# Kernel tuning notes

Measured on AMD Instinct MI355X. Metric: run time of the kernel, lower is better.

## Reference

```python
import jax, jax.numpy as jnp
import numpy as np

B = 1; T = 2048; H = 2048; NH = 16; KVH = 4; HD = 128; WIN = 512; SINK = 64
S = 64; NG = 4; MLP_I = 5504; CK = 4
INTER = NH * HD; CONV_DIM = INTER + 2 * NG * S; NPROJ = INTER + CONV_DIM + NH
EPS = 1e-6; MEPS = 1e-5


def rmsnorm(x, w, eps):
    return x * jax.lax.rsqrt(jnp.mean(x * x, -1, keepdims=True) + eps) * w


def rotate_half(x):
    h = x.shape[-1] // 2
    return jnp.concatenate([-x[..., h:], x[..., :h]], -1)


def setup_inputs():
    key = jax.random.key(0)
    ks = jax.random.split(key, 32)
    rn = lambda k, s, sc=0.02: jax.random.normal(k, s, dtype=jnp.float32) * sc
    inv = 1.0 / (10000.0 ** (np.arange(0, HD, 2, dtype=np.float64) / HD))
    fr = np.outer(np.arange(T), inv)
    emb = np.concatenate([fr, fr], -1)
    return {
        'hidden_states': jax.random.normal(ks[0], (B, T, H), dtype=jnp.float32),
        'cos': jnp.asarray(np.cos(emb), jnp.float32)[None],
        'sin': jnp.asarray(np.sin(emb), jnp.float32)[None],
        'ln1_w': jnp.ones((H,), jnp.float32),
        'q_w': rn(ks[1], (NH * HD, H)), 'q_b': rn(ks[2], (NH * HD,)),
        'k_w': rn(ks[3], (KVH * HD, H)), 'k_b': rn(ks[4], (KVH * HD,)),
        'v_w': rn(ks[5], (KVH * HD, H)), 'v_b': rn(ks[6], (KVH * HD,)),
        'o_w': rn(ks[7], (H, NH * HD)),
        'in_proj_w': rn(ks[8], (NPROJ, H)),
        'conv_w': rn(ks[9], (CONV_DIM, 1, CK), 0.1),
        'conv_b': rn(ks[10], (CONV_DIM,), 0.1),
        'dt_bias': rn(ks[11], (NH,), 0.5),
        'A_log': rn(ks[12], (NH,), 0.5),
        'D': rn(ks[13], (NH,), 0.5),
        'mnorm_w': jnp.ones((INTER,), jnp.float32),
        'out_proj_w': rn(ks[14], (H, INTER)),
        'ln2_w': jnp.ones((H,), jnp.float32),
        'gate_w': rn(ks[15], (MLP_I, H)),
        'up_w': rn(ks[16], (MLP_I, H)),
        'down_w': rn(ks[17], (H, MLP_I)),
    }


def _mamba2(ev, in_proj_w, conv_w, conv_b, dt_bias, A_log, D, mnorm_w, out_proj_w):
    # ev: [B, L, H] evicted hidden states; Mamba2 with expand=1 (intermediate=INTER)
    L = ev.shape[1]
    proj = jnp.einsum('blh,ph->blp', ev, in_proj_w)
    z = proj[..., :INTER]
    xBC = proj[..., INTER:INTER + CONV_DIM]
    dt = proj[..., INTER + CONV_DIM:]
    # depthwise causal conv1d, kernel 4
    xBC = jax.lax.conv_general_dilated(
        xBC.transpose(0, 2, 1), conv_w, (1,), [(CK - 1, 0)],
        dimension_numbers=('NCH', 'OIH', 'NCH'), feature_group_count=CONV_DIM)
    xBC = jax.nn.silu((xBC + conv_b[None, :, None]).transpose(0, 2, 1))
    x = xBC[..., :INTER].reshape(B, L, NH, HD)
    Bm = jnp.repeat(xBC[..., INTER:INTER + NG * S].reshape(B, L, NG, S), NH // NG, axis=2)
    Cm = jnp.repeat(xBC[..., INTER + NG * S:].reshape(B, L, NG, S), NH // NG, axis=2)
    dt = jax.nn.softplus(dt + dt_bias)  # [B, L, NH]
    A = -jnp.exp(A_log)  # [NH]

    def scan_one(xb, bb, cb, db):
        def step(state, inp):
            xt, bt, ct, dtt = inp  # [NH,HD],[NH,S],[NH,S],[NH]
            decay = jnp.exp(dtt * A)[:, None, None]
            state = decay * state + (dtt[:, None] * xt)[..., None] * bt[:, None, :]
            y = jnp.einsum('hds,hs->hd', state, ct) + D[:, None] * xt
            return state, y
        _, ys = jax.lax.scan(step, jnp.zeros((NH, HD, S), xb.dtype), (xb, bb, cb, db))
        return ys

    y = jax.vmap(scan_one)(x, Bm, Cm, dt).reshape(B, L, INTER)
    g = y * jax.nn.silu(z)  # gated RMSNorm
    g = g * jax.lax.rsqrt(jnp.mean(g * g, -1, keepdims=True) + MEPS) * mnorm_w
    return jnp.einsum('bli,hi->blh', g, out_proj_w)


def reference(hidden_states, cos, sin, ln1_w, q_w, q_b, k_w, k_b, v_w, v_b, o_w,
              in_proj_w, conv_w, conv_b, dt_bias, A_log, D, mnorm_w, out_proj_w,
              ln2_w, gate_w, up_w, down_w):
    pre = rmsnorm(hidden_states, ln1_w, EPS)  # input_layernorm
    evict_end = T - WIN
    mem_out = _mamba2(pre[:, SINK:evict_end, :], in_proj_w, conv_w, conv_b,
                      dt_bias, A_log, D, mnorm_w, out_proj_w)  # [B, Le, H]
    mem_act = mem_out[:, -1:, :]

    def qkv(x, w, b, nh):
        return (jnp.einsum('blh,ph->blp', x, w) + b).reshape(x.shape[0], x.shape[1], nh, HD).transpose(0, 2, 1, 3)

    q = qkv(pre, q_w, q_b, NH)
    k = qkv(pre, k_w, k_b, KVH)
    v = qkv(pre, v_w, v_b, KVH)
    c = cos[:, None]; s = sin[:, None]
    q = q * c + rotate_half(q) * s
    k = k * c + rotate_half(k) * s
    # mem token injection at position SINK (mem projections are not rotated)
    q = q.at[:, :, SINK, :].set(qkv(mem_act, q_w, q_b, NH)[:, :, 0, :])
    k = k.at[:, :, SINK, :].set(qkv(mem_act, k_w, k_b, KVH)[:, :, 0, :])
    v = v.at[:, :, SINK, :].set(qkv(mem_act, v_w, v_b, KVH)[:, :, 0, :])
    # sink + sliding-window causal mask with mem-token bias
    row = jnp.arange(T)[:, None]; col = jnp.arange(T)[None, :]
    protected = SINK + 1
    bad = (col > row) | ((col < row - WIN) & (col >= protected))
    minv = jnp.finfo(jnp.float32).min
    mask = jnp.where(bad, minv, 0.0)[None, None]
    le_fact = (T - SINK - WIN) / T
    mask = mask.at[..., SINK].add(0.5 * le_fact)
    rep = NH // KVH
    kf = jnp.repeat(k, rep, axis=1)
    vf = jnp.repeat(v, rep, axis=1)
    scores = jnp.einsum('bhqd,bhkd->bhqk', q, kf) * (HD ** -0.5) + mask
    attn = jax.nn.softmax(scores, axis=-1)
    o = jnp.einsum('bhqk,bhkd->bhqd', attn, vf).transpose(0, 2, 1, 3).reshape(B, T, NH * HD)
    # training-path merge: sinks | mem_out | window
    merged = jnp.concatenate([o[:, :SINK], mem_out, o[:, T - WIN:]], axis=1)
    attn_out = jnp.einsum('blp,hp->blh', merged, o_w)
    h = hidden_states + attn_out
    m = rmsnorm(h, ln2_w, EPS)
    mlp = jnp.einsum('bli,hi->blh',
                     jax.nn.silu(jnp.einsum('blh,ih->bli', m, gate_w)) * jnp.einsum('blh,ih->bli', m, up_w),
                     down_w)
    return h + mlp
```

## Files before the change

### kernel.cpp

```cpp
#include <hip/hip_runtime.h>
#include <hip/hip_bf16.h>

#define TSEQ   2048
#define HDIM   2048
#define NHEAD  16
#define KVHEAD 4
#define HEADD  128
#define WINSZ  512
#define SINKN  64
#define MLPI   5504
#define CONVD  2560
#define NPROJD 4624
#define LMEM   1472
#define NCHUNK 23
#define QKVD   3072

typedef unsigned short bf_t;
typedef __attribute__((ext_vector_type(8))) short short8;
typedef __attribute__((ext_vector_type(4))) short s4v;
typedef __attribute__((ext_vector_type(4))) float ffrag;

#define BOF_PRE   0ull
#define BOF_QKV   8388608ull
#define BOF_P     8388608ull
#define BOF_S     20447232ull
#define BOF_PROJ  33554432ull
#define BOF_GB    33554432ull
#define BOF_XBCC  60780544ull
#define BOF_GF    75853824ull
#define BOF_MERG  75853824ull
#define BOF_GN    87912448ull
#define BOF_H     93941760ull
#define BOF_DT    110718976ull
#define BOF_GA    110813184ull
#define BOF_FLAG  110907392ull
#define BOF_LC    110908416ull

#define BOF_CNV_A 8388608ull
#define BOF_CNV_B 60780544ull

__device__ __forceinline__ float bf2f(bf_t x) { return __uint_as_float(((unsigned)x) << 16); }
__device__ __forceinline__ bf_t f2bf(float x) {
  unsigned u = __float_as_uint(x);
  return (bf_t)((u + 0x7FFFu + ((u >> 16) & 1u)) >> 16);
}
__device__ __forceinline__ float ldin(const void* p, size_t i, int bf) {
  if (bf) return bf2f(((const bf_t*)p)[i]);
  return ((const float*)p)[i];
}
__device__ __forceinline__ float siluf(float x) { return x / (1.f + expf(-x)); }

typedef const __attribute__((address_space(1))) unsigned gl_u32;
typedef __attribute__((address_space(3))) unsigned lds_u32;
__device__ __forceinline__ void gld16(const void* g, void* l) {
  __builtin_amdgcn_global_load_lds((gl_u32*)g, (lds_u32*)l, 16, 0, 0);
}

__device__ __forceinline__ void xcd_swz(int gx, int gy, int& x, int& y) {
  int id = blockIdx.y * gx + blockIdx.x;
  int total = gx * gy;
  int xcd = id & 7, j = id >> 3;
  int q = total >> 3, r = total & 7;
  int w = (xcd < r ? xcd*(q+1) : r*(q+1) + (xcd-r)*q) + j;
  x = w / gy;
  y = w % gy;
}

__global__ void detect_k(const void* __restrict__ ln1, int* __restrict__ flag) {
  unsigned w0 = *(const unsigned*)ln1;
  *flag = (w0 == 0x3F803F80u) ? 1 : 0;
}

__global__ __launch_bounds__(256) void wconv_k(const float* __restrict__ src,
    bf_t* __restrict__ dst, int n8, const int* __restrict__ flagp) {
  if (*flagp) return;
  int idx = blockIdx.x*256 + threadIdx.x;
  if (idx >= n8) return;
  const float* s = src + (size_t)idx*8;
  float4 a = *(const float4*)s, b = *(const float4*)(s+4);
  short8 o;
  o[0]=(short)f2bf(a.x); o[1]=(short)f2bf(a.y); o[2]=(short)f2bf(a.z); o[3]=(short)f2bf(a.w);
  o[4]=(short)f2bf(b.x); o[5]=(short)f2bf(b.y); o[6]=(short)f2bf(b.z); o[7]=(short)f2bf(b.w);
  *(short8*)(dst + (size_t)idx*8) = o;
}

__global__ __launch_bounds__(256) void rms_in_k(const void* __restrict__ x,
    const void* __restrict__ w, bf_t* __restrict__ out, float eps,
    const int* __restrict__ flagp) {
  int bf = *flagp;
  int row = blockIdx.x, tid = threadIdx.x;
  float v[8];
  if (bf) {
    const bf_t* xr = (const bf_t*)x + (size_t)row*HDIM + tid*8;
#pragma unroll
    for (int j = 0; j < 8; ++j) v[j] = bf2f(xr[j]);
  } else {
    const float* xr = (const float*)x + (size_t)row*HDIM + tid*8;
    float4 a = *(const float4*)xr, b = *(const float4*)(xr+4);
    v[0]=a.x; v[1]=a.y; v[2]=a.z; v[3]=a.w; v[4]=b.x; v[5]=b.y; v[6]=b.z; v[7]=b.w;
  }
  float ss = 0.f;
#pragma unroll
  for (int j = 0; j < 8; ++j) ss += v[j]*v[j];
  __shared__ float red[256];
  red[tid] = ss; __syncthreads();
  for (int s = 128; s > 0; s >>= 1) { if (tid < s) red[tid] += red[tid+s]; __syncthreads(); }
  float scale = 1.f / sqrtf(red[0]*(1.f/HDIM) + eps);
  bf_t* o = out + (size_t)row*HDIM + tid*8;
#pragma unroll
  for (int j = 0; j < 8; ++j) o[j] = f2bf(v[j]*scale*ldin(w, tid*8+j, bf));
}

__global__ __launch_bounds__(256) void rms_f2b_k(const float* __restrict__ x,
    const void* __restrict__ w, bf_t* __restrict__ out, float eps,
    const int* __restrict__ flagp) {
  int bf = *flagp;
  int row = blockIdx.x, tid = threadIdx.x;
  const float* xr = x + (size_t)row*2048 + tid*8;
  float4 a = *(const float4*)xr, b = *(const float4*)(xr+4);
  float v[8] = {a.x,a.y,a.z,a.w,b.x,b.y,b.z,b.w};
  float ss = 0.f;
#pragma unroll
  for (int j = 0; j < 8; ++j) ss += v[j]*v[j];
  __shared__ float red[256];
  red[tid] = ss; __syncthreads();
  for (int s = 128; s > 0; s >>= 1) { if (tid < s) red[tid] += red[tid+s]; __syncthreads(); }
  float scale = 1.f / sqrtf(red[0]*(1.f/2048.f) + eps);
  bf_t* o = out + (size_t)row*2048 + tid*8;
#pragma unroll
  for (int j = 0; j < 8; ++j) o[j] = f2bf(v[j]*scale*ldin(w, tid*8+j, bf));
}

__global__ __launch_bounds__(256) void tgemm_k(
    const bf_t* __restrict__ A, int lda,
    const void* __restrict__ W0, const void* __restrict__ W1, const void* __restrict__ W2,
    const bf_t* __restrict__ C0, const bf_t* __restrict__ C1, const bf_t* __restrict__ C2,
    int ldw, int n1, int n2,
    const void* __restrict__ b0, const void* __restrict__ b1, const void* __restrict__ b2,
    const void* __restrict__ res,
    const float* __restrict__ hf,
    void* __restrict__ out,
    int ldc, int M, int N, int K, int mode, int outbf,
    const int* __restrict__ flagp) {
  int bf = *flagp;
  __shared__ short As[8192];
  __shared__ short Bs[4096];
  int tid = threadIdx.x;
  int lane = tid & 63, wv = tid >> 6;
  int sx, sy; xcd_swz(gridDim.x, gridDim.y, sx, sy);
  int bm = sy << 7, bn = sx << 6;

  int trow = tid >> 2;
  int kc = (((tid & 3) ^ ((tid >> 3) & 3)) << 3);
  int ar0 = bm + trow;        if (ar0 > M-1) ar0 = M-1;
  int ar1 = bm + 64 + trow;   if (ar1 > M-1) ar1 = M-1;
  int wr  = bn + trow;        if (wr > N-1) wr = N-1;
  const bf_t* ga0 = A + (size_t)ar0*lda + kc;
  const bf_t* ga1 = A + (size_t)ar1*lda + kc;
  const bf_t* w0 = bf ? (const bf_t*)W0 : C0;
  const bf_t* w1 = bf ? (const bf_t*)W1 : C1;
  const bf_t* w2 = bf ? (const bf_t*)W2 : C2;
  const bf_t* Wsel; int wrl;
  if (wr < n1)      { Wsel = w0; wrl = wr; }
  else if (wr < n2) { Wsel = w1; wrl = wr - n1; }
  else              { Wsel = w2; wrl = wr - n2; }
  const bf_t* gwb = Wsel + (size_t)wrl*ldw + kc;
  int sA = wv*512;

  int wm = (wv & 1) << 6, wn = (wv >> 1) << 5;
  int fr = lane & 15;
  int fq = (((lane >> 4) ^ ((fr >> 1) & 3)) << 3);

  ffrag acc[4][2];
#pragma unroll
  for (int i = 0; i < 4; ++i)
#pragma unroll
    for (int j = 0; j < 2; ++j) acc[i][j] = (ffrag){0.f,0.f,0.f,0.f};

  gld16(ga0, As + sA);
  gld16(ga1, As + 2048 + sA);
  gld16(gwb, Bs + sA);
  __syncthreads();

  int cur = 0;
  for (int k0 = 0; k0 < K; k0 += 32) {
    int nxt = k0 + 32;
    int nb = (cur ^ 1) << 12;
    int nbB = (cur ^ 1) << 11;
    if (nxt < K) {
      gld16(ga0 + nxt, As + nb + sA);
      gld16(ga1 + nxt, As + nb + 2048 + sA);
      gld16(gwb + nxt, Bs + nbB + sA);
    }
    int cbA = cur << 12, cbB = cur << 11;
    short8 af[4], bfr[2];
#pragma unroll
    for (int i = 0; i < 4; ++i)
      af[i] = *(const short8*)&As[cbA + (wm + i*16 + fr)*32 + fq];
#pragma unroll
    for (int j = 0; j < 2; ++j)
      bfr[j] = *(const short8*)&Bs[cbB + (wn + j*16 + fr)*32 + fq];
#pragma unroll
    for (int i = 0; i < 4; ++i)
#pragma unroll
      for (int j = 0; j < 2; ++j)
        acc[i][j] = __builtin_amdgcn_mfma_f32_16x16x32_bf16(af[i], bfr[j], acc[i][j], 0, 0, 0);
    __syncthreads();
    cur ^= 1;
  }

  int rbase = (lane >> 4) << 2;
  int cbase = lane & 15;
#pragma unroll
  for (int i = 0; i < 4; ++i) {
#pragma unroll
    for (int j = 0; j < 2; ++j) {
#pragma unroll
      for (int r = 0; r < 4; ++r) {
        int m = bm + wm + i*16 + rbase + r;
        int n = bn + wn + j*16 + cbase;
        if (m >= M || n >= N) continue;
        size_t ci = (size_t)m*ldc + n;
        float v = acc[i][j][r];
        if (mode == 0) {
          if (b0) {
            if (n < n1)      v += ldin(b0, n, bf);
            else if (n < n2) v += ldin(b1, n - n1, bf);
            else             v += ldin(b2, n - n2, bf);
          }
          if (outbf) ((bf_t*)out)[ci] = f2bf(v); else ((float*)out)[ci] = v;
        } else if (mode == 1) {
          ((float*)out)[ci] = v + ldin(res, ci, bf);
        } else {
          float hv = hf[ci] + v;
          if (bf) ((bf_t*)out)[ci] = f2bf(hv); else ((float*)out)[ci] = hv;
        }
      }
    }
  }
}

__global__ __launch_bounds__(256, 2) void fgemm_k(
    const bf_t* __restrict__ A, int lda,
    const void* __restrict__ Wg, const void* __restrict__ Wu,
    const bf_t* __restrict__ Cg, const bf_t* __restrict__ Cu, int ldw,
    bf_t* __restrict__ out, int M, int N, int K,
    const int* __restrict__ flagp) {
  int bf = *flagp;
  __shared__ short As[8192];
  __shared__ short Bg[8192];
  __shared__ short Bu[8192];
  int tid = threadIdx.x;
  int lane = tid & 63, wv = tid >> 6;
  int sx, sy; xcd_swz(gridDim.x, gridDim.y, sx, sy);
  int bm = sy << 7, bn = sx << 7;

  int trow = tid >> 2;
  int kc = (((tid & 3) ^ ((tid >> 3) & 3)) << 3);
  int ar0 = bm + trow;        if (ar0 > M-1) ar0 = M-1;
  int ar1 = bm + 64 + trow;   if (ar1 > M-1) ar1 = M-1;
  const bf_t* ga0 = A + (size_t)ar0*lda + kc;
  const bf_t* ga1 = A + (size_t)ar1*lda + kc;
  const bf_t* wg = bf ? (const bf_t*)Wg : Cg;
  const bf_t* wu = bf ? (const bf_t*)Wu : Cu;
  const bf_t* gg0 = wg + (size_t)(bn + trow)*ldw + kc;
  const bf_t* gg1 = wg + (size_t)(bn + 64 + trow)*ldw + kc;
  const bf_t* gu0 = wu + (size_t)(bn + trow)*ldw + kc;
  const bf_t* gu1 = wu + (size_t)(bn + 64 + trow)*ldw + kc;
  int sA = wv*512;

  int wm = (wv & 1) << 6, wn = (wv >> 1) << 6;
  int fr = lane & 15;
  int fq = (((lane >> 4) ^ ((fr >> 1) & 3)) << 3);

  ffrag ag[4][4], au[4][4];
#pragma unroll
  for (int i = 0; i < 4; ++i)
#pragma unroll
    for (int j = 0; j < 4; ++j) { ag[i][j] = (ffrag){0.f,0.f,0.f,0.f}; au[i][j] = (ffrag){0.f,0.f,0.f,0.f}; }

  gld16(ga0, As + sA);
  gld16(ga1, As + 2048 + sA);
  gld16(gg0, Bg + sA);
  gld16(gg1, Bg + 2048 + sA);
  gld16(gu0, Bu + sA);
  gld16(gu1, Bu + 2048 + sA);
  __syncthreads();

  int cur = 0;
  for (int k0 = 0; k0 < K; k0 += 32) {
    int nxt = k0 + 32;
    int nb = (cur ^ 1) << 12;
    if (nxt < K) {
      gld16(ga0 + nxt, As + nb + sA);
      gld16(ga1 + nxt, As + nb + 2048 + sA);
      gld16(gg0 + nxt, Bg + nb + sA);
      gld16(gg1 + nxt, Bg + nb + 2048 + sA);
      gld16(gu0 + nxt, Bu + nb + sA);
      gld16(gu1 + nxt, Bu + nb + 2048 + sA);
    }
    int cb = cur << 12;
    short8 af[4], bgf[4], buf2[4];
#pragma unroll
    for (int i = 0; i < 4; ++i)
      af[i] = *(const short8*)&As[cb + (wm + i*16 + fr)*32 + fq];
#pragma unroll
    for (int j = 0; j < 4; ++j) {
      bgf[j]  = *(const short8*)&Bg[cb + (wn + j*16 + fr)*32 + fq];
      buf2[j] = *(const short8*)&Bu[cb + (wn + j*16 + fr)*32 + fq];
    }
#pragma unroll
    for (int i = 0; i < 4; ++i)
#pragma unroll
      for (int j = 0; j < 4; ++j) {
        ag[i][j] = __builtin_amdgcn_mfma_f32_16x16x32_bf16(af[i], bgf[j],  ag[i][j], 0, 0, 0);
        au[i][j] = __builtin_amdgcn_mfma_f32_16x16x32_bf16(af[i], buf2[j], au[i][j], 0, 0, 0);
      }
    __syncthreads();
    cur ^= 1;
  }

  int rbase = (lane >> 4) << 2;
  int cbase = lane & 15;
#pragma unroll
  for (int i = 0; i < 4; ++i)
#pragma unroll
    for (int j = 0; j < 4; ++j)
#pragma unroll
      for (int r = 0; r < 4; ++r) {
        int m = bm + wm + i*16 + rbase + r;
        int n = bn + wn + j*16 + cbase;
        if (m >= M || n >= N) continue;
        float g = ag[i][j][r], u = au[i][j][r];
        out[(size_t)m*N + n] = f2bf(siluf(g) * u);
      }
}

__global__ __launch_bounds__(256) void rope_k(float* __restrict__ tb, int stride,
    const void* __restrict__ cosp, const void* __restrict__ sinp,
    int nheads, const int* __restrict__ flagp) {
  int bf = *flagp;
  int idx = blockIdx.x*256 + threadIdx.x;
  int d = idx & 63;
  int rem = idx >> 6;
  int tpos = rem / nheads, hh = rem % nheads;
  float* base = tb + (size_t)tpos*stride + hh*128;
  float a = base[d], b = base[d+64];
  float c0 = ldin(cosp, (size_t)tpos*128 + d, bf),    s0 = ldin(sinp, (size_t)tpos*128 + d, bf);
  float c1 = ldin(cosp, (size_t)tpos*128 + d + 64, bf), s1 = ldin(sinp, (size_t)tpos*128 + d + 64, bf);
  base[d]    = a*c0 - b*s0;
  base[d+64] = b*c1 + a*s1;
}

__global__ __launch_bounds__(256) void conv_k(const float* __restrict__ proj,
    const void* __restrict__ convw, const void* __restrict__ convb,
    float* __restrict__ xbcc, const int* __restrict__ flagp) {
  int bf = *flagp;
  int idx = blockIdx.x*256 + threadIdx.x;
  int t = idx / CONVD, c = idx % CONVD;
  float acc = ldin(convb, c, bf);
#pragma unroll
  for (int j = 0; j < 4; ++j) {
    int tt = t - 3 + j;
    if (tt >= 0) acc += ldin(convw, (size_t)c*4 + j, bf) * proj[(size_t)tt*NPROJD + 2048 + c];
  }
  xbcc[idx] = siluf(acc);
}

__global__ __launch_bounds__(256) void dt_k(const float* __restrict__ proj,
    const void* __restrict__ dtb, const void* __restrict__ alog,
    float* __restrict__ dtv, float* __restrict__ ga, const int* __restrict__ flagp) {
  int bf = *flagp;
  int idx = blockIdx.x*256 + threadIdx.x;
  int t = idx >> 4, h = idx & 15;
  float raw = proj[(size_t)t*NPROJD + 4608 + h] + ldin(dtb, h, bf);
  float dt = (raw > 30.f) ? raw : log1pf(expf(raw));
  float A = -expf(ldin(alog, h, bf));
  dtv[idx] = dt;
  ga[idx] = dt*A;
}

__global__ __launch_bounds__(256) void cums_k(const float* __restrict__ ga,
    float* __restrict__ Lc) {
  int wid = blockIdx.x*4 + (threadIdx.x >> 6);
  int lane = threadIdx.x & 63;
  int h = wid / NCHUNK, c = wid % NCHUNK;
  int t = c*64 + lane;
  float a = ga[(size_t)t*16 + h];
#pragma unroll
  for (int off = 1; off < 64; off <<= 1) {
    float o = __shfl_up(a, off, 64);
    if (lane >= off) a += o;
  }
  Lc[(size_t)(h*NCHUNK + c)*64 + lane] = a;
}

__global__ __launch_bounds__(256) void chunkstate_k(
    const float* __restrict__ xbcc, const float* __restrict__ dtv,
    const float* __restrict__ Lc, float* __restrict__ Pbuf) {
  __shared__ short XT[128*72];
  __shared__ short BT[64*72];
  __shared__ float wj[64];
  int tid = threadIdx.x, lane = tid & 63, wv = tid >> 6;
  int b = blockIdx.x;
  int h = b & 15, c = b >> 4;
  int g64 = (h >> 2) << 6;
  size_t hc = (size_t)(h*NCHUNK + c);

  if (tid < 64) {
    float L63 = Lc[hc*64 + 63];
    float Lj  = Lc[hc*64 + tid];
    wj[tid] = dtv[(size_t)(c*64 + tid)*16 + h] * expf(L63 - Lj);
  }
  __syncthreads();
  for (int base = tid*4; base < 8192; base += 1024) {
    int j = base >> 7, d = base & 127;
    float4 xv = *(const float4*)&xbcc[(size_t)(c*64 + j)*CONVD + h*128 + d];
    XT[(d+0)*72 + j] = (short)f2bf(xv.x);
    XT[(d+1)*72 + j] = (short)f2bf(xv.y);
    XT[(d+2)*72 + j] = (short)f2bf(xv.z);
    XT[(d+3)*72 + j] = (short)f2bf(xv.w);
  }
  for (int base = tid*4; base < 4096; base += 1024) {
    int j = base >> 6, s = base & 63;
    float w = wj[j];
    float4 bv = *(const float4*)&xbcc[(size_t)(c*64 + j)*CONVD + 2048 + g64 + s];
    BT[(s+0)*72 + j] = (short)f2bf(bv.x * w);
    BT[(s+1)*72 + j] = (short)f2bf(bv.y * w);
    BT[(s+2)*72 + j] = (short)f2bf(bv.z * w);
    BT[(s+3)*72 + j] = (short)f2bf(bv.w * w);
  }
  __syncthreads();

  int fr = lane & 15, fq = (lane >> 4) << 3;
  ffrag acc[2][4];
#pragma unroll
  for (int i = 0; i < 2; ++i)
#pragma unroll
    for (int j = 0; j < 4; ++j) acc[i][j] = (ffrag){0.f,0.f,0.f,0.f};
#pragma unroll
  for (int k0 = 0; k0 < 64; k0 += 32) {
    short8 af[2], bfr[4];
#pragma unroll
    for (int i = 0; i < 2; ++i)
      af[i] = *(const short8*)&XT[(wv*32 + i*16 + fr)*72 + k0 + fq];
#pragma unroll
    for (int j = 0; j < 4; ++j)
      bfr[j] = *(const short8*)&BT[(j*16 + fr)*72 + k0 + fq];
#pragma unroll
    for (int i = 0; i < 2; ++i)
#pragma unroll
      for (int j = 0; j < 4; ++j)
        acc[i][j] = __builtin_amdgcn_mfma_f32_16x16x32_bf16(af[i], bfr[j], acc[i][j], 0, 0, 0);
  }
  int rbase = (lane >> 4) << 2, cbase = lane & 15;
#pragma unroll
  for (int i = 0; i < 2; ++i)
#pragma unroll
    for (int j = 0; j < 4; ++j)
#pragma unroll
      for (int r = 0; r < 4; ++r) {
        int d = wv*32 + i*16 + rbase + r;
        int s = j*16 + cbase;
        Pbuf[hc*8192 + d*64 + s] = acc[i][j][r];
      }
}

__global__ __launch_bounds__(256) void statepass_k(
    const float* __restrict__ Pbuf, const float* __restrict__ Lc,
    float* __restrict__ Sbuf) {
  int gid = blockIdx.x*256 + threadIdx.x;
  int h = gid >> 13, rem = gid & 8191;
  float s = 0.f;
  for (int c = 0; c < NCHUNK; ++c) {
    size_t hc = (size_t)(h*NCHUNK + c);
    Sbuf[hc*8192 + rem] = s;
    s = expf(Lc[hc*64 + 63]) * s + Pbuf[hc*8192 + rem];
  }
}

__global__ __launch_bounds__(256) void chunkout_k(
    const float* __restrict__ xbcc, const float* __restrict__ proj,
    const float* __restrict__ dtv, const float* __restrict__ Lc,
    const float* __restrict__ Sbuf, const void* __restrict__ Dp,
    float* __restrict__ g, const int* __restrict__ flagp) {
  __shared__ short Cs[64*72];
  __shared__ short BsS[64*72];
  __shared__ short XT[128*72];
  __shared__ short Sinb[128*72];
  __shared__ float Lch[64];
  __shared__ float dtch[64];
  int bf = *flagp;
  int tid = threadIdx.x, lane = tid & 63, wv = tid >> 6;
  int b = blockIdx.x;
  int h = b & 15, c = b >> 4;
  int g64 = (h >> 2) << 6;
  size_t hc = (size_t)(h*NCHUNK + c);
  float Dh = ldin(Dp, h, bf);

  if (tid < 64) {
    Lch[tid]  = Lc[hc*64 + tid];
    dtch[tid] = dtv[(size_t)(c*64 + tid)*16 + h];
  }
  for (int base = tid*4; base < 4096; base += 1024) {
    int i = base >> 6, s = base & 63;
    float4 cv = *(const float4*)&xbcc[(size_t)(c*64 + i)*CONVD + 2304 + g64 + s];
    Cs[i*72 + s+0] = (short)f2bf(cv.x); Cs[i*72 + s+1] = (short)f2bf(cv.y);
    Cs[i*72 + s+2] = (short)f2bf(cv.z); Cs[i*72 + s+3] = (short)f2bf(cv.w);
    float4 bv = *(const float4*)&xbcc[(size_t)(c*64 + i)*CONVD + 2048 + g64 + s];
    BsS[i*72 + s+0] = (short)f2bf(bv.x); BsS[i*72 + s+1] = (short)f2bf(bv.y);
    BsS[i*72 + s+2] = (short)f2bf(bv.z); BsS[i*72 + s+3] = (short)f2bf(bv.w);
  }
  for (int base = tid*4; base < 8192; base += 1024) {
    int j = base >> 7, d = base & 127;
    float4 xv = *(const float4*)&xbcc[(size_t)(c*64 + j)*CONVD + h*128 + d];
    XT[(d+0)*72 + j] = (short)f2bf(xv.x);
    XT[(d+1)*72 + j] = (short)f2bf(xv.y);
    XT[(d+2)*72 + j] = (short)f2bf(xv.z);
    XT[(d+3)*72 + j] = (short)f2bf(xv.w);
  }
  for (int base = tid*4; base < 8192; base += 1024) {
    int d = base >> 6, s = base & 63;
    float4 sv = *(const float4*)&Sbuf[hc*8192 + d*64 + s];
    Sinb[d*72 + s+0] = (short)f2bf(sv.x); Sinb[d*72 + s+1] = (short)f2bf(sv.y);
    Sinb[d*72 + s+2] = (short)f2bf(sv.z); Sinb[d*72 + s+3] = (short)f2bf(sv.w);
  }
  __syncthreads();

  int fr = lane & 15, fq = (lane >> 4) << 3;
  ffrag s0[4];
#pragma unroll
  for (int i = 0; i < 4; ++i) s0[i] = (ffrag){0.f,0.f,0.f,0.f};
#pragma unroll
  for (int k0 = 0; k0 < 64; k0 += 32) {
    short8 bfr = *(const short8*)&BsS[(wv*16 + fr)*72 + k0 + fq];
#pragma unroll
    for (int i = 0; i < 4; ++i) {
      short8 af = *(const short8*)&Cs[(i*16 + fr)*72 + k0 + fq];
      s0[i] = __builtin_amdgcn_mfma_f32_16x16x32_bf16(af, bfr, s0[i], 0, 0, 0);
    }
  }
  __syncthreads();

  {
    int rbase = (lane >> 4) << 2, cbase = lane & 15;
    int j = wv*16 + cbase;
#pragma unroll
    for (int i = 0; i < 4; ++i)
#pragma unroll
      for (int r = 0; r < 4; ++r) {
        int ii = i*16 + rbase + r;
        float v = (j <= ii) ? s0[i][r] * expf(Lch[ii] - Lch[j]) * dtch[j] : 0.f;
        BsS[ii*72 + j] = (short)f2bf(v);
      }
#pragma unroll
    for (int e = 0; e < 16; ++e) {
      int idx = tid*16 + e;
      int ii = idx >> 6, s = idx & 63;
      Cs[ii*72 + s] = (short)f2bf(bf2f((bf_t)Cs[ii*72 + s]) * expf(Lch[ii]));
    }
  }
  __syncthreads();

  ffrag acc[4][2];
#pragma unroll
  for (int i = 0; i < 4; ++i)
#pragma unroll
    for (int j = 0; j < 2; ++j) acc[i][j] = (ffrag){0.f,0.f,0.f,0.f};
#pragma unroll
  for (int k0 = 0; k0 < 64; k0 += 32) {
    short8 xb[2], af[4];
#pragma unroll
    for (int j = 0; j < 2; ++j)
      xb[j] = *(const short8*)&XT[(wv*32 + j*16 + fr)*72 + k0 + fq];
#pragma unroll
    for (int i = 0; i < 4; ++i)
      af[i] = *(const short8*)&BsS[(i*16 + fr)*72 + k0 + fq];
#pragma unroll
    for (int i = 0; i < 4; ++i)
#pragma unroll
      for (int j = 0; j < 2; ++j)
        acc[i][j] = __builtin_amdgcn_mfma_f32_16x16x32_bf16(af[i], xb[j], acc[i][j], 0, 0, 0);
  }
#pragma unroll
  for (int k0 = 0; k0 < 64; k0 += 32) {
    short8 sb[2], af[4];
#pragma unroll
    for (int j = 0; j < 2; ++j)
      sb[j] = *(const short8*)&Sinb[(wv*32 + j*16 + fr)*72 + k0 + fq];
#pragma unroll
    for (int i = 0; i < 4; ++i)
      af[i] = *(const short8*)&Cs[(i*16 + fr)*72 + k0 + fq];
#pragma unroll
    for (int i = 0; i < 4; ++i)
#pragma unroll
      for (int j = 0; j < 2; ++j)
        acc[i][j] = __builtin_amdgcn_mfma_f32_16x16x32_bf16(af[i], sb[j], acc[i][j], 0, 0, 0);
  }

  int rbase = (lane >> 4) << 2, cbase = lane & 15;
#pragma unroll
  for (int i = 0; i < 4; ++i)
#pragma unroll
    for (int j = 0; j < 2; ++j)
#pragma unroll
      for (int r = 0; r < 4; ++r) {
        int ii = i*16 + rbase + r;
        int d = wv*32 + j*16 + cbase;
        int t = c*64 + ii;
        int col = h*128 + d;
        float x = xbcc[(size_t)t*CONVD + col];
        float z = proj[(size_t)t*NPROJD + col];
        float y = acc[i][j][r] + Dh*x;
        g[(size_t)t*2048 + col] = y * siluf(z);
      }
}

__global__ __launch_bounds__(256) void memact_k(
    const bf_t* __restrict__ merged,
    const void* __restrict__ qw, const void* __restrict__ qb,
    const void* __restrict__ kw, const void* __restrict__ kb,
    const void* __restrict__ vw, const void* __restrict__ vb,
    const bf_t* __restrict__ cq, const bf_t* __restrict__ ck, const bf_t* __restrict__ cv,
    float* __restrict__ qkv, const int* __restrict__ flagp) {
  int bf = *flagp;
  int p = blockIdx.x, tid = threadIdx.x;
  const bf_t* ma = merged + (size_t)1535*2048;
  const void* b; const bf_t* wb; int off;
  if (p < 2048)      { wb = bf ? (const bf_t*)qw : cq; b = qb; off = p; }
  else if (p < 2560) { wb = bf ? (const bf_t*)kw : ck; b = kb; off = p - 2048; }
  else               { wb = bf ? (const bf_t*)vw : cv; b = vb; off = p - 2560; }
  float partial = 0.f;
  size_t wbase = (size_t)off*2048;
  for (int j = tid; j < 2048; j += 256) partial += bf2f(ma[j])*bf2f(wb[wbase + j]);
  __shared__ float red[256];
  red[tid] = partial; __syncthreads();
  for (int s = 128; s > 0; s >>= 1) { if (tid < s) red[tid] += red[tid+s]; __syncthreads(); }
  if (tid == 0) qkv[(size_t)64*QKVD + p] = red[0] + ldin(b, off, bf);
}

__global__ __launch_bounds__(256) void attn3_k(
    const float* __restrict__ qkv, bf_t* __restrict__ merged) {
  __shared__ short Qs[64*136];
  __shared__ short Ks[64*136];
  __shared__ short Vt[128*72];
  __shared__ short Pb[64*72];

  int bid = blockIdx.x;
  int g = bid & 3, hg = (bid >> 2) & 3, qt = bid >> 4;
  int r0 = (qt == 0) ? 0 : (1536 + 64*(qt-1));
  int tid = threadIdx.x, lane = tid & 63, wv = tid >> 6;

  int qcol = g*512 + hg*128;
  int kcol = 2048 + g*128;
  int vcol = 2560 + g*128;

  int fr = lane & 15, fq = (lane >> 4) << 3;
  int rloc = (lane >> 4) << 2;
  int cb = lane & 15;

  {
    int row = tid >> 2, c4 = tid & 3;
    const float* qp = qkv + (size_t)(r0 + row)*QKVD + qcol;
#pragma unroll
    for (int rep = 0; rep < 8; ++rep) {
      int d = (c4 + rep*4)*4;
      float4 v = *(const float4*)(qp + d);
      s4v o;
      o[0] = (short)f2bf(v.x); o[1] = (short)f2bf(v.y);
      o[2] = (short)f2bf(v.z); o[3] = (short)f2bf(v.w);
      *(s4v*)&Qs[row*136 + d] = o;
    }
  }
  __syncthreads();

  float m4[4] = {-3.0e38f, -3.0e38f, -3.0e38f, -3.0e38f};
  float l4[4] = {0.f, 0.f, 0.f, 0.f};
  ffrag o8[8];
#pragma unroll
  for (int n = 0; n < 8; ++n) o8[n] = (ffrag){0.f,0.f,0.f,0.f};

  int ntiles = (qt == 0) ? 1 : 11;
  for (int t = 0; t < ntiles; ++t) {
    int kb = (t == 0) ? 0 : ((t == 1) ? 64 : (r0 - 512 + 64*(t-2)));

    {
      int row = tid >> 2, c4 = tid & 3;
      const float* kp = qkv + (size_t)(kb + row)*QKVD + kcol;
#pragma unroll
      for (int rep = 0; rep < 8; ++rep) {
        int d = (c4 + rep*4)*4;
        float4 v = *(const float4*)(kp + d);
        s4v o;
        o[0] = (short)f2bf(v.x); o[1] = (short)f2bf(v.y);
        o[2] = (short)f2bf(v.z); o[3] = (short)f2bf(v.w);
        *(s4v*)&Ks[row*136 + d] = o;
      }
    }
#pragma unroll
    for (int it = 0; it < 8; ++it) {
      int task = tid + it*256;
      int d = task & 127, jg = task >> 7;
      const float* vp = qkv + (size_t)(kb + jg*4)*QKVD + vcol + d;
      s4v o;
      o[0] = (short)f2bf(vp[0]);
      o[1] = (short)f2bf(vp[QKVD]);
      o[2] = (short)f2bf(vp[2*QKVD]);
      o[3] = (short)f2bf(vp[3*QKVD]);
      *(s4v*)&Vt[d*72 + jg*4] = o;
    }
    __syncthreads();

    ffrag s[4];
#pragma unroll
    for (int n = 0; n < 4; ++n) s[n] = (ffrag){0.f,0.f,0.f,0.f};
#pragma unroll
    for (int k0 = 0; k0 < 128; k0 += 32) {
      short8 aq = *(const short8*)&Qs[(wv*16 + fr)*136 + k0 + fq];
#pragma unroll
      for (int n = 0; n < 4; ++n) {
        short8 bk = *(const short8*)&Ks[(n*16 + fr)*136 + k0 + fq];
        s[n] = __builtin_amdgcn_mfma_f32_16x16x32_bf16(aq, bk, s[n], 0, 0, 0);
      }
    }

    float tmax[4] = {-INFINITY, -INFINITY, -INFINITY, -INFINITY};
#pragma unroll
    for (int n = 0; n < 4; ++n) {
      int kk = kb + n*16 + cb;
      float bias = (kk == 64) ? 0.359375f : 0.f;
#pragma unroll
      for (int rg = 0; rg < 4; ++rg) {
        int rr = r0 + wv*16 + rloc + rg;
        bool ok = (kk <= rr) && ((kk >= rr - 512) || (kk < 65));
        float sv = ok ? (s[n][rg]*0.08838834764831845f + bias) : -INFINITY;
        s[n][rg] = sv;
        tmax[rg] = fmaxf(tmax[rg], sv);
      }
    }
    float sc4[4];
#pragma unroll
    for (int rg = 0; rg < 4; ++rg) {
#pragma unroll
      for (int off = 1; off < 16; off <<= 1)
        tmax[rg] = fmaxf(tmax[rg], __shfl_xor(tmax[rg], off, 64));
      float mnew = fmaxf(m4[rg], tmax[rg]);
      sc4[rg] = expf(m4[rg] - mnew);
      m4[rg] = mnew;
      l4[rg] *= sc4[rg];
    }
#pragma unroll
    for (int n = 0; n < 8; ++n)
#pragma unroll
      for (int rg = 0; rg < 4; ++rg) o8[n][rg] *= sc4[rg];

    float ts[4] = {0.f, 0.f, 0.f, 0.f};
#pragma unroll
    for (int n = 0; n < 4; ++n)
#pragma unroll
      for (int rg = 0; rg < 4; ++rg) {
        float p = expf(s[n][rg] - m4[rg]);
        ts[rg] += p;
        Pb[(wv*16 + rloc + rg)*72 + n*16 + cb] = (short)f2bf(p);
      }
#pragma unroll
    for (int rg = 0; rg < 4; ++rg) {
#pragma unroll
      for (int off = 1; off < 16; off <<= 1) ts[rg] += __shfl_xor(ts[rg], off, 64);
      l4[rg] += ts[rg];
    }

#pragma unroll
    for (int k0 = 0; k0 < 64; k0 += 32) {
      short8 ap = *(const short8*)&Pb[(wv*16 + fr)*72 + k0 + fq];
#pragma unroll
      for (int n = 0; n < 8; ++n) {
        short8 bv = *(const short8*)&Vt[(n*16 + fr)*72 + k0 + fq];
        o8[n] = __builtin_amdgcn_mfma_f32_16x16x32_bf16(ap, bv, o8[n], 0, 0, 0);
      }
    }
    __syncthreads();
  }

  float inv[4];
#pragma unroll
  for (int rg = 0; rg < 4; ++rg) inv[rg] = 1.f / l4[rg];
#pragma unroll
  for (int n = 0; n < 8; ++n)
#pragma unroll
    for (int rg = 0; rg < 4; ++rg) {
      int i = wv*16 + rloc + rg;
      int d = n*16 + cb;
      merged[(size_t)(r0 + i)*2048 + (g*4 + hg)*128 + d] = f2bf(o8[n][rg]*inv[rg]);
    }
}

extern "C" void kernel_launch(void* const* d_in, const int* in_sizes, int n_in,
                              void* d_out, int out_size, void* d_ws, size_t ws_size,
                              hipStream_t stream) {
  const void* hidden = d_in[0];
  const void* cosp   = d_in[1];
  const void* sinp   = d_in[2];
  const void* ln1w   = d_in[3];
  const void* qw = d_in[4];  const void* qb = d_in[5];
  const void* kw = d_in[6];  const void* kb = d_in[7];
  const void* vw = d_in[8];  const void* vb = d_in[9];
  const void* ow = d_in[10];
  const void* inpw = d_in[11];
  const void* convw = d_in[12]; const void* convb = d_in[13];
  const void* dtb = d_in[14]; const void* alog = d_in[15]; const void* dd = d_in[16];
  const void* mnw = d_in[17]; const void* outpw = d_in[18];
  const void* ln2w = d_in[19];
  const void* gatew = d_in[20]; const void* upw = d_in[21]; const void* downw = d_in[22];

  char* wsb = (char*)d_ws;
  bf_t*  pre    = (bf_t*)(wsb + BOF_PRE);
  bf_t*  mbuf   = (bf_t*)(wsb + BOF_PRE);
  float* qkv    = (float*)(wsb + BOF_QKV);
  float* Pbuf   = (float*)(wsb + BOF_P);
  float* Sbuf   = (float*)(wsb + BOF_S);
  float* proj   = (float*)(wsb + BOF_PROJ);
  bf_t*  Gbuf   = (bf_t*)(wsb + BOF_GB);
  float* xbcc   = (float*)(wsb + BOF_XBCC);
  float* gbuf   = (float*)(wsb + BOF_GF);
  bf_t*  merged = (bf_t*)(wsb + BOF_MERG);
  bf_t*  gn     = (bf_t*)(wsb + BOF_GN);
  float* hbuf   = (float*)(wsb + BOF_H);
  float* dtv    = (float*)(wsb + BOF_DT);
  float* ga     = (float*)(wsb + BOF_GA);
  int*   flag   = (int*)(wsb + BOF_FLAG);
  float* Lc     = (float*)(wsb + BOF_LC);
  bf_t*  cvA    = (bf_t*)(wsb + BOF_CNV_A);
  bf_t*  cvB    = (bf_t*)(wsb + BOF_CNV_B);
  bf_t*  cvq    = cvB;
  bf_t*  cvk    = cvB + 4194304;
  bf_t*  cvv    = cvB + 5242880;

  detect_k<<<dim3(1), dim3(1), 0, stream>>>(ln1w, flag);
  rms_in_k<<<dim3(TSEQ), dim3(256), 0, stream>>>(hidden, ln1w, pre, 1e-6f, flag);

  wconv_k<<<dim3(4624), dim3(256), 0, stream>>>((const float*)inpw, cvA, 1183744, flag);
  tgemm_k<<<dim3(73,12), dim3(256), 0, stream>>>(pre + (size_t)64*2048, 2048,
      inpw, nullptr, nullptr, cvA, nullptr, nullptr, 2048, NPROJD, NPROJD,
      nullptr, nullptr, nullptr,
      nullptr, nullptr, proj, NPROJD, LMEM, NPROJD, 2048, 0, 0, flag);
  conv_k<<<dim3((LMEM*CONVD)/256), dim3(256), 0, stream>>>(proj, convw, convb, xbcc, flag);
  dt_k<<<dim3((LMEM*16)/256), dim3(256), 0, stream>>>(proj, dtb, alog, dtv, ga, flag);
  cums_k<<<dim3(92), dim3(256), 0, stream>>>(ga, Lc);
  chunkstate_k<<<dim3(368), dim3(256), 0, stream>>>(xbcc, dtv, Lc, Pbuf);
  statepass_k<<<dim3(512), dim3(256), 0, stream>>>(Pbuf, Lc, Sbuf);
  wconv_k<<<dim3(2048), dim3(256), 0, stream>>>((const float*)outpw, cvA, 524288, flag);
  chunkout_k<<<dim3(368), dim3(256), 0, stream>>>(xbcc, proj, dtv, Lc, Sbuf, dd, gbuf, flag);
  rms_f2b_k<<<dim3(LMEM), dim3(256), 0, stream>>>(gbuf, mnw, gn, 1e-5f, flag);
  tgemm_k<<<dim3(32,12), dim3(256), 0, stream>>>(gn, 2048,
      outpw, nullptr, nullptr, cvA, nullptr, nullptr, 2048, 2048, 2048,
      nullptr, nullptr, nullptr,
      nullptr, nullptr, merged + (size_t)64*2048, 2048, LMEM, 2048, 2048, 0, 1, flag);

  wconv_k<<<dim3(2048), dim3(256), 0, stream>>>((const float*)qw, cvq, 524288, flag);
  wconv_k<<<dim3(512),  dim3(256), 0, stream>>>((const float*)kw, cvk, 131072, flag);
  wconv_k<<<dim3(512),  dim3(256), 0, stream>>>((const float*)vw, cvv, 131072, flag);
  tgemm_k<<<dim3(48,16), dim3(256), 0, stream>>>(pre, 2048,
      qw, kw, vw, cvq, cvk, cvv, 2048, 2048, 2560, qb, kb, vb,
      nullptr, nullptr, qkv, QKVD, 2048, QKVD, 2048, 0, 0, flag);
  rope_k<<<dim3(8192), dim3(256), 0, stream>>>(qkv, QKVD, cosp, sinp, 16, flag);
  rope_k<<<dim3(2048), dim3(256), 0, stream>>>(qkv + 2048, QKVD, cosp, sinp, 4, flag);

  memact_k<<<dim3(3072), dim3(256), 0, stream>>>(merged, qw, qb, kw, kb, vw, vb,
      cvq, cvk, cvv, qkv, flag);
  attn3_k<<<dim3(144), dim3(256), 0, stream>>>(qkv, merged);

  wconv_k<<<dim3(2048), dim3(256), 0, stream>>>((const float*)ow, cvB, 524288, flag);
  tgemm_k<<<dim3(32,16), dim3(256), 0, stream>>>(merged, 2048,
      ow, nullptr, nullptr, cvB, nullptr, nullptr, 2048, 2048, 2048,
      nullptr, nullptr, nullptr,
      hidden, nullptr, hbuf, 2048, 2048, 2048, 2048, 1, 0, flag);
  rms_f2b_k<<<dim3(TSEQ), dim3(256), 0, stream>>>(hbuf, ln2w, mbuf, 1e-6f, flag);

  wconv_k<<<dim3(5504), dim3(256), 0, stream>>>((const float*)gatew, cvA, 1409024, flag);
  wconv_k<<<dim3(5504), dim3(256), 0, stream>>>((const float*)upw,   cvB, 1409024, flag);
  fgemm_k<<<dim3(43,16), dim3(256), 0, stream>>>(mbuf, 2048, gatew, upw, cvA, cvB, 2048,
      Gbuf, 2048, MLPI, 2048, flag);
  wconv_k<<<dim3(5504), dim3(256), 0, stream>>>((const float*)downw, cvA, 1409024, flag);
  tgemm_k<<<dim3(32,16), dim3(256), 0, stream>>>(Gbuf, MLPI,
      downw, nullptr, nullptr, cvA, nullptr, nullptr, MLPI, 2048, 2048,
      nullptr, nullptr, nullptr,
      nullptr, hbuf, d_out, 2048, 2048, 2048, MLPI, 3, 0, flag);
}
```

Measured before the change: 664.0 us.

## Deepen GEMM global-to-LDS prefetch to two stages with explicit waitcnt barriers

Restructures the main GEMM and the fused gate/up GEMM loops so two K-tiles are in flight. Each iteration waits with partial vmcnt and a raw s_barrier, reads fragments from LDS, then issues the direct-to-LDS load for tile t+2 into the buffer just consumed, ahead of the MFMAs. This replaces the __syncthreads-based single-tile lookahead so global load latency overlaps more compute. It relies on gld16 being a direct LDS load counted by vmcnt, and on K being a multiple of 32 with at least two tiles.

Measured after the change: 628.4 us (median of 2 runs). 1.06x faster.

```diff
diff --git a/kernel.cpp b/kernel.cpp
--- a/kernel.cpp
+++ b/kernel.cpp
@@ -177,22 +177,19 @@
 #pragma unroll
     for (int j = 0; j < 2; ++j) acc[i][j] = (ffrag){0.f,0.f,0.f,0.f};
 
+  int nst = K >> 5;
   gld16(ga0, As + sA);
   gld16(ga1, As + 2048 + sA);
   gld16(gwb, Bs + sA);
-  __syncthreads();
-
-  int cur = 0;
-  for (int k0 = 0; k0 < K; k0 += 32) {
-    int nxt = k0 + 32;
-    int nb = (cur ^ 1) << 12;
-    int nbB = (cur ^ 1) << 11;
-    if (nxt < K) {
-      gld16(ga0 + nxt, As + nb + sA);
-      gld16(ga1 + nxt, As + nb + 2048 + sA);
-      gld16(gwb + nxt, Bs + nbB + sA);
-    }
-    int cbA = cur << 12, cbB = cur << 11;
+  gld16(ga0 + 32, As + 4096 + sA);
+  gld16(ga1 + 32, As + 4096 + 2048 + sA);
+  gld16(gwb + 32, Bs + 2048 + sA);
+
+  for (int t = 0; t < nst; ++t) {
+    if (t + 1 < nst) { asm volatile("s_waitcnt vmcnt(3)" ::: "memory"); }
+    else             { asm volatile("s_waitcnt vmcnt(0)" ::: "memory"); }
+    __builtin_amdgcn_s_barrier();
+    int cbA = (t & 1) << 12, cbB = (t & 1) << 11;
     short8 af[4], bfr[2];
 #pragma unroll
     for (int i = 0; i < 4; ++i)
@@ -200,13 +197,19 @@
 #pragma unroll
     for (int j = 0; j < 2; ++j)
       bfr[j] = *(const short8*)&Bs[cbB + (wn + j*16 + fr)*32 + fq];
+    asm volatile("s_waitcnt lgkmcnt(0)" ::: "memory");
+    __builtin_amdgcn_s_barrier();
+    int nxt = (t + 2) << 5;
+    if (nxt < K) {
+      gld16(ga0 + nxt, As + cbA + sA);
+      gld16(ga1 + nxt, As + cbA + 2048 + sA);
+      gld16(gwb + nxt, Bs + cbB + sA);
+    }
 #pragma unroll
     for (int i = 0; i < 4; ++i)
 #pragma unroll
       for (int j = 0; j < 2; ++j)
         acc[i][j] = __builtin_amdgcn_mfma_f32_16x16x32_bf16(af[i], bfr[j], acc[i][j], 0, 0, 0);
-    __syncthreads();
-    cur ^= 1;
   }
 
   int rbase = (lane >> 4) << 2;
@@ -279,27 +282,25 @@
 #pragma unroll
     for (int j = 0; j < 4; ++j) { ag[i][j] = (ffrag){0.f,0.f,0.f,0.f}; au[i][j] = (ffrag){0.f,0.f,0.f,0.f}; }
 
+  int nst = K >> 5;
   gld16(ga0, As + sA);
   gld16(ga1, As + 2048 + sA);
   gld16(gg0, Bg + sA);
   gld16(gg1, Bg + 2048 + sA);
   gld16(gu0, Bu + sA);
   gld16(gu1, Bu + 2048 + sA);
-  __syncthreads();
-
-  int cur = 0;
-  for (int k0 = 0; k0 < K; k0 += 32) {
-    int nxt = k0 + 32;
-    int nb = (cur ^ 1) << 12;
-    if (nxt < K) {
-      gld16(ga0 + nxt, As + nb + sA);
-      gld16(ga1 + nxt, As + nb + 2048 + sA);
-      gld16(gg0 + nxt, Bg + nb + sA);
-      gld16(gg1 + nxt, Bg + nb + 2048 + sA);
-      gld16(gu0 + nxt, Bu + nb + sA);
-      gld16(gu1 + nxt, Bu + nb + 2048 + sA);
-    }
-    int cb = cur << 12;
+  gld16(ga0 + 32, As + 4096 + sA);
+  gld16(ga1 + 32, As + 4096 + 2048 + sA);
+  gld16(gg0 + 32, Bg + 4096 + sA);
+  gld16(gg1 + 32, Bg + 4096 + 2048 + sA);
+  gld16(gu0 + 32, Bu + 4096 + sA);
+  gld16(gu1 + 32, Bu + 4096 + 2048 + sA);
+
+  for (int t = 0; t < nst; ++t) {
+    if (t + 1 < nst) { asm volatile("s_waitcnt vmcnt(6)" ::: "memory"); }
+    else             { asm volatile("s_waitcnt vmcnt(0)" ::: "memory"); }
+    __builtin_amdgcn_s_barrier();
+    int cb = (t & 1) << 12;
     short8 af[4], bgf[4], buf2[4];
 #pragma unroll
     for (int i = 0; i < 4; ++i)
@@ -309,6 +310,17 @@
       bgf[j]  = *(const short8*)&Bg[cb + (wn + j*16 + fr)*32 + fq];
       buf2[j] = *(const short8*)&Bu[cb + (wn + j*16 + fr)*32 + fq];
     }
+    asm volatile("s_waitcnt lgkmcnt(0)" ::: "memory");
+    __builtin_amdgcn_s_barrier();
+    int nxt = (t + 2) << 5;
+    if (nxt < K) {
+      gld16(ga0 + nxt, As + cb + sA);
+      gld16(ga1 + nxt, As + cb + 2048 + sA);
+      gld16(gg0 + nxt, Bg + cb + sA);
+      gld16(gg1 + nxt, Bg + cb + 2048 + sA);
+      gld16(gu0 + nxt, Bu + cb + sA);
+      gld16(gu1 + nxt, Bu + cb + 2048 + sA);
+    }
 #pragma unroll
     for (int i = 0; i < 4; ++i)
 #pragma unroll
@@ -316,8 +328,6 @@
         ag[i][j] = __builtin_amdgcn_mfma_f32_16x16x32_bf16(af[i], bgf[j],  ag[i][j], 0, 0, 0);
         au[i][j] = __builtin_amdgcn_mfma_f32_16x16x32_bf16(af[i], buf2[j], au[i][j], 0, 0, 0);
       }
-    __syncthreads();
-    cur ^= 1;
   }
 
   int rbase = (lane >> 4) << 2;
```
